# Performance work log

Measured on AMD Instinct MI355X. Metric: run time of the kernel, lower is better.

The kernel has to match this reference:

```python
import jax, jax.numpy as jnp
import numpy as np

HID, NH, HD = 1024, 16, 64
B, S = 2, 2048


def _gammas(nh):
    # gammas = 1 - exp(linspace(log(1/512), log(1/32), nh))
    lin = np.linspace(np.log(1.0 / 512.0), np.log(1.0 / 32.0), nh)
    return jnp.asarray(1.0 - np.exp(lin), dtype=jnp.float32)


def setup_inputs() -> dict:
    key = jax.random.key(0)
    ks = jax.random.split(key, 6)
    x = jax.random.normal(ks[0], (B, S, HID), dtype=jnp.float32)
    # Per-head retention projection weights (Retention has its own q/k/v of [head_size, head_size])
    wq = jax.random.normal(ks[1], (NH, HD, HD), dtype=jnp.float32) / HD
    wk = jax.random.normal(ks[2], (NH, HD, HD), dtype=jnp.float32) / HD
    wv = jax.random.normal(ks[3], (NH, HD, HD), dtype=jnp.float32) / HD
    w1 = jax.random.normal(ks[4], (HID, HID), dtype=jnp.float32) / HID
    w2 = jax.random.normal(ks[5], (HID, HID), dtype=jnp.float32) / HID
    gn_scale = jnp.ones((HID,), dtype=jnp.float32)
    gn_bias = jnp.zeros((HID,), dtype=jnp.float32)
    return {"x": x, "wq": wq, "wk": wk, "wv": wv, "w1": w1, "w2": w2,
            "gn_scale": gn_scale, "gn_bias": gn_bias}


def reference(x, wq, wk, wv, w1, w2, gn_scale, gn_bias):
    b, s, h = x.shape
    nh, hd = wq.shape[0], wq.shape[1]
    gammas = _gammas(nh)  # [nh]

    xh = x.reshape(b, s, nh, hd)
    q = jnp.einsum('bsnd,nde->bsne', xh, wq)
    k = jnp.einsum('bsnd,nde->bsne', xh, wk)
    v = jnp.einsum('bsnd,nde->bsne', xh, wv)

    # causal decay mask D[n, s, t] = gamma_n ** (s - t) for s >= t else 0
    idx = jnp.arange(s)
    diff = (idx[:, None] - idx[None, :]).astype(jnp.float32)  # [s, s]
    safe = jnp.maximum(diff, 0.0)
    D = jnp.where(diff >= 0,
                  jnp.exp(safe[None] * jnp.log(gammas)[:, None, None]),
                  0.0)  # [nh, s, s]

    scores = jnp.einsum('bsnd,btnd->bnst', q, k) * D[None]      # [b, nh, s, s]
    ret = jnp.einsum('bnst,btnd->bsnd', scores, v)              # [b, s, nh, hd]

    # GroupNorm(num_groups=nh, num_channels=h) over flattened [b*s, h]:
    # normalize within each head-group of hd channels, affine per-channel, eps=1e-5
    mean = ret.mean(axis=-1, keepdims=True)
    var = ret.var(axis=-1, keepdims=True)
    norm = (ret - mean) / jnp.sqrt(var + 1e-5)
    norm = norm.reshape(b, s, h) * gn_scale + gn_bias

    gate = jnp.matmul(x, w1)
    out = gate * jax.nn.sigmoid(gate) + norm  # swish-gated branch + retention
    return jnp.matmul(out, w2)
```

## Files before the change

kernel.cpp:

```cpp
#include <hip/hip_runtime.h>

#define HIDD 1024
#define NHH  16
#define HDD  64
#define BBB  2
#define SSS  2048
#define BS   (BBB * SSS)

typedef __attribute__((ext_vector_type(8))) _Float16 half8;
typedef __attribute__((ext_vector_type(4))) _Float16 half4;
typedef __attribute__((ext_vector_type(4))) float    f32x4;

#define LSCALE 2048.0f
#define LINV   (1.0f / 2048.0f)

static __device__ __forceinline__ f32x4 mfma16h(half8 a, half8 b, f32x4 c) {
    return __builtin_amdgcn_mfma_f32_16x16x32_f16(a, b, c, 0, 0, 0);
}

static __device__ __forceinline__ void split2h(float v, _Float16& h, _Float16& l) {
    h = (_Float16)v;
    l = (_Float16)((v - (float)h) * LSCALE);
}

static __device__ __forceinline__ void gl_lds16(const _Float16* g, _Float16* l) {
    __builtin_amdgcn_global_load_lds(
        (const __attribute__((address_space(1))) unsigned int*)g,
        (__attribute__((address_space(3))) unsigned int*)l,
        16, 0, 0);
}

__global__ __launch_bounds__(256) void k_wprep(const float* __restrict__ wq,
                                               const float* __restrict__ wk,
                                               const float* __restrict__ wv,
                                               _Float16* __restrict__ WTh,
                                               _Float16* __restrict__ WTl) {
    const int blk = blockIdx.x;
    const int mat = blk >> 4, n = blk & 15;
    const float* src = (mat == 0 ? wq : mat == 1 ? wk : wv) + (size_t)n * 4096;
    for (int c = threadIdx.x; c < 4096; c += 256) {
        int e = c >> 6, d = c & 63;
        float v = src[d * 64 + e];
        _Float16 h, l;
        split2h(v, h, l);
        WTh[(size_t)blk * 4096 + c] = h;
        WTl[(size_t)blk * 4096 + c] = l;
    }
}

__global__ __launch_bounds__(512) void k_proj_mfma(const float* __restrict__ x,
                                                   const _Float16* __restrict__ WTh,
                                                   const _Float16* __restrict__ WTl,
                                                   _Float16* __restrict__ Qh, _Float16* __restrict__ Ql,
                                                   _Float16* __restrict__ Kh, _Float16* __restrict__ Kl,
                                                   _Float16* __restrict__ VTh, _Float16* __restrict__ VTl) {
    const int n  = blockIdx.y;
    const int R0 = blockIdx.x * 128;
    const int tid = threadIdx.x;
    const int w = tid >> 6, lane = tid & 63;
    const int hi = lane >> 4, lo = lane & 15;

    __shared__ __align__(16) _Float16 smem[27648];

    half8 ah[2], al[2];
#pragma unroll
    for (int kf = 0; kf < 2; kf++) {
        const float* xp = x + (size_t)(R0 + 16 * w + lo) * HIDD + n * HDD + kf * 32 + 8 * hi;
        float4 v0 = *(const float4*)xp;
        float4 v1 = *(const float4*)(xp + 4);
        float vv[8] = { v0.x, v0.y, v0.z, v0.w, v1.x, v1.y, v1.z, v1.w };
#pragma unroll
        for (int j = 0; j < 8; ++j) {
            _Float16 h, l;
            split2h(vv[j], h, l);
            ah[kf][j] = h; al[kf][j] = l;
        }
    }

    for (int c = tid; c < 3072; c += 512) {
        int m = c >> 10, rest = c & 1023, hl = rest >> 9, cc = rest & 511;
        int r = cc >> 3, j8 = (cc & 7) << 3;
        const _Float16* src = (hl ? WTl : WTh) + ((size_t)(m * NHH + n)) * 4096 + r * 64 + j8;
        *(half8*)&smem[(m * 2 + hl) * 4608 + r * 72 + j8] = *(const half8*)src;
    }
    __syncthreads();

    const int bq = R0 >> 11;
    const int sr = R0 & 2047;
    const size_t bn = (size_t)(bq * NHH + n);
    float vkeep[4][4][2];

    for (int mat = 0; mat < 3; ++mat) {
        const _Float16* bh_base = smem + (mat * 2 + 0) * 4608;
        const _Float16* bl_base = smem + (mat * 2 + 1) * 4608;
        f32x4 a0[4], a1[4];
#pragma unroll
        for (int eb = 0; eb < 4; ++eb) {
            a0[eb] = (f32x4){0.f, 0.f, 0.f, 0.f};
            a1[eb] = (f32x4){0.f, 0.f, 0.f, 0.f};
        }
#pragma unroll
        for (int eb = 0; eb < 4; ++eb) {
            half8 bh0 = *(const half8*)&bh_base[(16 * eb + lo) * 72 + 8 * hi];
            half8 bh1 = *(const half8*)&bh_base[(16 * eb + lo) * 72 + 32 + 8 * hi];
            half8 bl0 = *(const half8*)&bl_base[(16 * eb + lo) * 72 + 8 * hi];
            half8 bl1 = *(const half8*)&bl_base[(16 * eb + lo) * 72 + 32 + 8 * hi];
            a0[eb] = mfma16h(ah[0], bh0, a0[eb]);
            a0[eb] = mfma16h(ah[1], bh1, a0[eb]);
            a1[eb] = mfma16h(ah[0], bl0, a1[eb]);
            a1[eb] = mfma16h(al[0], bh0, a1[eb]);
            a1[eb] = mfma16h(ah[1], bl1, a1[eb]);
            a1[eb] = mfma16h(al[1], bh1, a1[eb]);
        }

        if (mat < 2) {
            _Float16* Dh = (mat == 0) ? Qh : Kh;
            _Float16* Dl = (mat == 0) ? Ql : Kl;
#pragma unroll
            for (int eb = 0; eb < 4; ++eb)
#pragma unroll
                for (int r = 0; r < 4; ++r) {
                    int gr = R0 + 16 * w + 4 * hi + r;
                    int s = gr & 2047;
                    float val = a0[eb][r] + a1[eb][r] * LINV;
                    _Float16 h, l;
                    split2h(val, h, l);
                    size_t idx = (bn * SSS + s) * HDD + 16 * eb + lo;
                    Dh[idx] = h; Dl[idx] = l;
                }
        } else {
#pragma unroll
            for (int eb = 0; eb < 4; ++eb)
#pragma unroll
                for (int r = 0; r < 4; ++r) {
                    vkeep[eb][r][0] = a0[eb][r];
                    vkeep[eb][r][1] = a1[eb][r];
                }
        }
    }

    __syncthreads();
    _Float16* tbh = smem;
    _Float16* tbl = smem + 8704;
#pragma unroll
    for (int eb = 0; eb < 4; ++eb)
#pragma unroll
        for (int r = 0; r < 4; ++r) {
            int rl = 16 * w + 4 * hi + r;
            int ch = 16 * eb + lo;
            _Float16 h, l;
            split2h(vkeep[eb][r][0] + vkeep[eb][r][1] * LINV, h, l);
            tbh[ch * 136 + rl] = h;
            tbl[ch * 136 + rl] = l;
        }
    __syncthreads();
    for (int c = tid; c < 1024; c += 512) {
        int ch = c >> 4, s8 = (c & 15) << 3;
        int a64 = s8 & 64;
        int s0 = s8 & 63;
        int basePerm = a64 + (s0 & 32) + ((s0 >> 3) & 3) * 4;
        const _Float16* th = &tbh[ch * 136];
        const _Float16* tl = &tbl[ch * 136];
        half4 h0 = *(const half4*)(th + basePerm);
        half4 h1 = *(const half4*)(th + basePerm + 16);
        half4 l0 = *(const half4*)(tl + basePerm);
        half4 l1 = *(const half4*)(tl + basePerm + 16);
        half8 oh = {h0[0], h0[1], h0[2], h0[3], h1[0], h1[1], h1[2], h1[3]};
        half8 ol = {l0[0], l0[1], l0[2], l0[3], l1[0], l1[1], l1[2], l1[3]};
        size_t gi = (bn * HDD + ch) * SSS + sr + s8;
        *(half8*)(VTh + gi) = oh;
        *(half8*)(VTl + gi) = ol;
    }
}

__global__ __launch_bounds__(256) void k_ret_mfma(const _Float16* __restrict__ Qh, const _Float16* __restrict__ Ql,
                                                  const _Float16* __restrict__ Kh, const _Float16* __restrict__ Kl,
                                                  const _Float16* __restrict__ VTh, const _Float16* __restrict__ VTl,
                                                  const float* __restrict__ gns,
                                                  const float* __restrict__ gnb,
                                                  float* __restrict__ normb) {
    const int n = blockIdx.y, b = blockIdx.z;
    const int qt = (n < 8) ? ((int)gridDim.x - 1 - (int)blockIdx.x) : (int)blockIdx.x;
    const int tid = threadIdx.x;
    const int w = tid >> 6, lane = tid & 63;
    const int hi = lane >> 4, lo = lane & 15;

    const double l512 = -6.2383246250395075;
    const double l32  = -3.4657359027997265;
    double lin = l512 + (double)n * (l32 - l512) / 15.0;
    float gamma = (float)(1.0 - exp(lin));
    float l2g = log2f(gamma);
    int dmax = (int)(16.0f / (-l2g)) + 1;

    const int qb = qt * 64;
    const int qw = qb + 16 * w;
    int stb_start = (qb > dmax) ? ((qb - dmax) >> 5) : 0;
    const int stb_end  = 2 * qt + 1;
    const int stb_diag = qw >> 5;

    const size_t bn = (size_t)(b * NHH + n);
    const _Float16* Qhp = Qh + bn * SSS * HDD;
    const _Float16* Qlp = Ql + bn * SSS * HDD;
    const _Float16* Khp = Kh + bn * SSS * HDD;
    const _Float16* Klp = Kl + bn * SSS * HDD;
    const _Float16* Vhp = VTh + bn * HDD * SSS;
    const _Float16* Vlp = VTl + bn * HDD * SSS;

    half8 qfh[2], qfl[2];
#pragma unroll
    for (int kf = 0; kf < 2; kf++) {
        size_t o = (size_t)(qw + lo) * HDD + kf * 32 + 8 * hi;
        qfh[kf] = *(const half8*)(Qhp + o);
        qfl[kf] = *(const half8*)(Qlp + o);
    }

    f32x4 acc0[4], acc1[4];
#pragma unroll
    for (int e = 0; e < 4; e++) {
        acc0[e] = (f32x4){0.f, 0.f, 0.f, 0.f};
        acc1[e] = (f32x4){0.f, 0.f, 0.f, 0.f};
    }

    __shared__ __align__(16) _Float16 ksh[4096];
    __shared__ __align__(16) _Float16 ksl[4096];
    __shared__ __align__(16) _Float16 vsh[4096];
    __shared__ __align__(16) _Float16 vsl[4096];

    const _Float16* sg = (w == 0) ? Khp : (w == 1) ? Klp : (w == 2) ? Vhp : Vlp;
    _Float16* slds = (w == 0) ? ksh : (w == 1) ? ksl : (w == 2) ? vsh : vsl;
    size_t goff;
    if (w < 2) goff = (size_t)(lane >> 3) * HDD + (size_t)((((lane & 7) ^ ((lane >> 3) & 7))) << 3);
    else       goff = (size_t)(lane >> 2) * SSS + (size_t)((((lane & 3) ^ ((lane >> 3) & 3))) << 3);

    auto issue = [&](int tbase, int pb) {
        _Float16* Lb = slds + pb * 2048;
        if (w < 2) {
#pragma unroll
            for (int i = 0; i < 4; ++i)
                gl_lds16(sg + (size_t)(tbase + 8 * i) * HDD + goff, Lb + i * 512);
        } else {
#pragma unroll
            for (int i = 0; i < 4; ++i)
                gl_lds16(sg + (size_t)(16 * i) * SSS + tbase + goff, Lb + i * 512);
        }
    };

    const int ks0 = ((hi ^ (lo & 7)) << 3);
    const int ks1 = (((4 + hi) ^ (lo & 7)) << 3);
    const int vs0 = ((hi ^ ((lo >> 1) & 3)) << 3);

    float ftile = exp2f((float)(qw + lo - stb_start * 32) * l2g);
    const float gi16   = exp2f(-16.0f * l2g);
    const float ginv32 = exp2f(-32.0f * l2g);
    float f4[4];
#pragma unroll
    for (int r = 0; r < 4; ++r) f4[r] = exp2f(-(float)(4 * hi + r) * l2g);

    int pb = 0;
    issue(stb_start * 32, 0);
    __syncthreads();

    for (int stb = stb_start; stb <= stb_end; ++stb) {
        const int tbase = stb * 32;
        if (stb < stb_end) issue(tbase + 32, pb ^ 1);

        const bool active = (tbase <= qw + 15) && (tbase + 31 >= qw - dmax);
        if (active) {
            const bool dm = (stb == stb_diag);
            const _Float16* kh_ = &ksh[pb * 2048];
            const _Float16* kl_ = &ksl[pb * 2048];
            const _Float16* vh_ = &vsh[pb * 2048];
            const _Float16* vl_ = &vsl[pb * 2048];
            _Float16 ph4[2][4], pl4[2][4];
#pragma unroll
            for (int tt = 0; tt < 2; ++tt) {
                int rb = (16 * tt + lo) * 64;
                half8 kh0 = *(const half8*)&kh_[rb + ks0];
                half8 kh1 = *(const half8*)&kh_[rb + ks1];
                half8 kl0 = *(const half8*)&kl_[rb + ks0];
                half8 kl1 = *(const half8*)&kl_[rb + ks1];
                f32x4 s0 = (f32x4){0.f, 0.f, 0.f, 0.f};
                f32x4 s1 = (f32x4){0.f, 0.f, 0.f, 0.f};
                s0 = mfma16h(kh0, qfh[0], s0);
                s0 = mfma16h(kh1, qfh[1], s0);
                s1 = mfma16h(kl0, qfh[0], s1);
                s1 = mfma16h(kh0, qfl[0], s1);
                s1 = mfma16h(kl1, qfh[1], s1);
                s1 = mfma16h(kh1, qfl[1], s1);
                const float g = tt ? ftile * gi16 : ftile;
#pragma unroll
                for (int r = 0; r < 4; r++) {
                    float p = (s0[r] + s1[r] * LINV) * (g * f4[r]);
                    if (dm) {
                        int diff = (qw + lo) - (tbase + 16 * tt + 4 * hi + r);
                        if (diff < 0) p = 0.0f;
                    }
                    split2h(p, ph4[tt][r], pl4[tt][r]);
                }
            }
            half8 pfh = (half8){ph4[0][0], ph4[0][1], ph4[0][2], ph4[0][3],
                                ph4[1][0], ph4[1][1], ph4[1][2], ph4[1][3]};
            half8 pfl = (half8){pl4[0][0], pl4[0][1], pl4[0][2], pl4[0][3],
                                pl4[1][0], pl4[1][1], pl4[1][2], pl4[1][3]};
#pragma unroll
            for (int e = 0; e < 4; e++) {
                int vb = (16 * e + lo) * 32 + vs0;
                half8 vh0 = *(const half8*)&vh_[vb];
                half8 vl0 = *(const half8*)&vl_[vb];
                acc0[e] = mfma16h(pfh, vh0, acc0[e]);
                acc1[e] = mfma16h(pfh, vl0, acc1[e]);
                acc1[e] = mfma16h(pfl, vh0, acc1[e]);
            }
        }
        ftile *= ginv32;
        __syncthreads();
        pb ^= 1;
    }

    f32x4 accf[4];
#pragma unroll
    for (int e = 0; e < 4; e++)
#pragma unroll
        for (int r = 0; r < 4; r++)
            accf[e][r] = acc0[e][r] + acc1[e][r] * LINV;

    float s[4], sq[4];
#pragma unroll
    for (int r = 0; r < 4; r++) {
        s[r] = 0.f; sq[r] = 0.f;
#pragma unroll
        for (int e = 0; e < 4; e++) { float v = accf[e][r]; s[r] += v; sq[r] += v * v; }
    }
#pragma unroll
    for (int mask = 1; mask < 16; mask <<= 1)
#pragma unroll
        for (int r = 0; r < 4; r++) {
            s[r]  += __shfl_xor(s[r],  mask);
            sq[r] += __shfl_xor(sq[r], mask);
        }
#pragma unroll
    for (int e = 0; e < 4; e++)
#pragma unroll
        for (int r = 0; r < 4; r++) {
            float mean = s[r] * (1.0f / 64.0f);
            float var  = sq[r] * (1.0f / 64.0f) - mean * mean;
            float rstd = rsqrtf(var + 1e-5f);
            int ch = 16 * e + lo;
            int sg2 = qw + 4 * hi + r;
            float nv = (accf[e][r] - mean) * rstd;
            nv = nv * gns[n * 64 + ch] + gnb[n * 64 + ch];
            normb[((size_t)b * SSS + sg2) * HIDD + n * 64 + ch] = nv;
        }
}

__global__ __launch_bounds__(256) void k_cvt_h(const float* __restrict__ src,
                                               _Float16* __restrict__ dst) {
    int i = blockIdx.x * 256 + threadIdx.x;
    float4 v = reinterpret_cast<const float4*>(src)[i];
    half4 o = { (_Float16)v.x, (_Float16)v.y, (_Float16)v.z, (_Float16)v.w };
    reinterpret_cast<half4*>(dst)[i] = o;
}

__global__ __launch_bounds__(256) void k_tr_h(const float* __restrict__ src,
                                              _Float16* __restrict__ dst,
                                              int K, int N) {
    __shared__ float ls[32][33];
    int kb = blockIdx.y * 32, nb = blockIdx.x * 32;
    int tx = threadIdx.x & 31, ty = threadIdx.x >> 5;
#pragma unroll
    for (int i = 0; i < 4; i++) {
        int r = ty + 8 * i;
        ls[r][tx] = src[(size_t)(kb + r) * N + nb + tx];
    }
    __syncthreads();
#pragma unroll
    for (int i = 0; i < 4; i++) {
        int r = ty + 8 * i;
        dst[(size_t)(nb + r) * K + kb + tx] = (_Float16)ls[tx][r];
    }
}

template <int MODE>
__global__ __launch_bounds__(256) void k_gemm_h(const _Float16* __restrict__ A,
                                                const _Float16* __restrict__ Bt,
                                                const float* __restrict__ normb,
                                                _Float16* __restrict__ Y,
                                                float* __restrict__ Out) {
    const int Rb = blockIdx.x * 128, Cb = blockIdx.y * 128;
    const int tid = threadIdx.x, w = tid >> 6, lane = tid & 63;
    const int hi = lane >> 4, lo = lane & 15;
    const int wm = w >> 1, wn = w & 1;

    __shared__ __align__(16) _Float16 as[128 * 40];
    __shared__ __align__(16) _Float16 bs[128 * 40];

    f32x4 acc[4][4];
#pragma unroll
    for (int m = 0; m < 4; m++)
#pragma unroll
        for (int nn = 0; nn < 4; nn++) acc[m][nn] = (f32x4){0.f, 0.f, 0.f, 0.f};

    half8 pre[4];
    auto g_issue = [&](int kk) {
#pragma unroll
        for (int i = 0; i < 4; ++i) {
            int c = tid + (i << 8);
            int which = c >> 9, cc = c & 511, row = cc >> 2, j8 = (cc & 3) << 3;
            const _Float16* src = (which == 0)
                ? A  + (size_t)(Rb + row) * HIDD + kk * 32 + j8
                : Bt + (size_t)(Cb + row) * HIDD + kk * 32 + j8;
            pre[i] = *(const half8*)src;
        }
    };
    auto g_commit = [&]() {
#pragma unroll
        for (int i = 0; i < 4; ++i) {
            int c = tid + (i << 8);
            int which = c >> 9, cc = c & 511, row = cc >> 2, j8 = (cc & 3) << 3;
            _Float16* dst = (which == 0) ? as : bs;
            *(half8*)&dst[row * 40 + j8] = pre[i];
        }
    };

    g_issue(0);
    g_commit();
    __syncthreads();

    for (int kk = 0; kk < 32; ++kk) {
        if (kk < 31) g_issue(kk + 1);
        half8 af[4], bf[4];
#pragma unroll
        for (int m = 0; m < 4; m++)
            af[m] = *(const half8*)&as[(64 * wm + 16 * m + lo) * 40 + 8 * hi];
#pragma unroll
        for (int nn = 0; nn < 4; nn++)
            bf[nn] = *(const half8*)&bs[(64 * wn + 16 * nn + lo) * 40 + 8 * hi];
#pragma unroll
        for (int m = 0; m < 4; m++)
#pragma unroll
            for (int nn = 0; nn < 4; nn++)
                acc[m][nn] = mfma16h(af[m], bf[nn], acc[m][nn]);
        __syncthreads();
        if (kk < 31) g_commit();
        __syncthreads();
    }

#pragma unroll
    for (int m = 0; m < 4; m++)
#pragma unroll
        for (int nn = 0; nn < 4; nn++)
#pragma unroll
            for (int r = 0; r < 4; r++) {
                int row = Rb + 64 * wm + 16 * m + 4 * hi + r;
                int col = Cb + 64 * wn + 16 * nn + lo;
                float v = acc[m][nn][r];
                size_t idx = (size_t)row * HIDD + col;
                if (MODE == 0) {
                    float sw = v / (1.0f + expf(-v));
                    float y = sw + normb[idx];
                    Y[idx] = (_Float16)y;
                } else {
                    Out[idx] = v;
                }
            }
}

extern "C" void kernel_launch(void* const* d_in, const int* in_sizes, int n_in,
                              void* d_out, int out_size, void* d_ws, size_t ws_size,
                              hipStream_t stream) {
    const float* x   = (const float*)d_in[0];
    const float* wq  = (const float*)d_in[1];
    const float* wk  = (const float*)d_in[2];
    const float* wv  = (const float*)d_in[3];
    const float* w1  = (const float*)d_in[4];
    const float* w2  = (const float*)d_in[5];
    const float* gns = (const float*)d_in[6];
    const float* gnb = (const float*)d_in[7];
    float* out = (float*)d_out;

    char* base = (char*)d_ws;
    size_t off = 0;
    auto carve = [&](size_t bytes) -> void* {
        void* p = base + off;
        off += (bytes + 255) & ~(size_t)255;
        return p;
    };
    _Float16* Qh  = (_Float16*)carve((size_t)BS * HIDD * 2);
    _Float16* Ql  = (_Float16*)carve((size_t)BS * HIDD * 2);
    _Float16* Kh  = (_Float16*)carve((size_t)BS * HIDD * 2);
    _Float16* Kl  = (_Float16*)carve((size_t)BS * HIDD * 2);
    _Float16* VTh = (_Float16*)carve((size_t)BS * HIDD * 2);
    _Float16* VTl = (_Float16*)carve((size_t)BS * HIDD * 2);
    float*    normb = (float*)carve((size_t)BS * HIDD * 4);
    _Float16* WTh = (_Float16*)normb;
    _Float16* WTl = WTh + (size_t)48 * 4096;
    _Float16* xh  = Qh;
    _Float16* w1t = Kh;
    _Float16* w2t = Kh + (size_t)HIDD * HIDD;
    _Float16* yh  = VTh;
    (void)ws_size; (void)in_sizes; (void)n_in; (void)out_size;

    k_wprep<<<48, 256, 0, stream>>>(wq, wk, wv, WTh, WTl);
    k_proj_mfma<<<dim3(BS / 128, NHH), 512, 0, stream>>>(x, WTh, WTl,
                                                         Qh, Ql, Kh, Kl, VTh, VTl);
    k_ret_mfma<<<dim3(SSS / 64, NHH, BBB), 256, 0, stream>>>(Qh, Ql, Kh, Kl, VTh, VTl,
                                                             gns, gnb, normb);
    k_cvt_h<<<(BS * HIDD) / 4 / 256, 256, 0, stream>>>(x, xh);
    k_tr_h<<<dim3(32, 32), 256, 0, stream>>>(w1, w1t, HIDD, HIDD);
    k_tr_h<<<dim3(32, 32), 256, 0, stream>>>(w2, w2t, HIDD, HIDD);
    k_gemm_h<0><<<dim3(BS / 128, HIDD / 128), 256, 0, stream>>>(xh, w1t, normb, yh, nullptr);
    k_gemm_h<1><<<dim3(BS / 128, HIDD / 128), 256, 0, stream>>>(yh, w2t, nullptr, nullptr, out);
}
```

Before: 168.9 us.

## Use direct global-to-LDS loads with XOR swizzle and BK=64 in fp16 GEMM

Replaces the register-staged global→LDS prefetch (issue/commit with padded 40-stride rows) with direct global-to-LDS 16-byte loads (gl_lds16), an XOR-swizzled unpadded 64-wide layout, and a doubled K tile of 64 per iteration. This is meant to cut register pressure, VGPR round-trips and loop iterations, and to avoid bank conflicts without padding. The trade-off is that the software prefetch overlap is lost: each iteration now syncs, loads, syncs, then computes, with no double-buffering.

```diff
diff --git a/kernel.cpp b/kernel.cpp
--- a/kernel.cpp
+++ b/kernel.cpp
@@ -391,8 +391,8 @@
     const int hi = lane >> 4, lo = lane & 15;
     const int wm = w >> 1, wn = w & 1;
 
-    __shared__ __align__(16) _Float16 as[128 * 40];
-    __shared__ __align__(16) _Float16 bs[128 * 40];
+    __shared__ __align__(16) _Float16 as[128 * 64];
+    __shared__ __align__(16) _Float16 bs[128 * 64];
 
     f32x4 acc[4][4];
 #pragma unroll
@@ -400,49 +400,45 @@
 #pragma unroll
         for (int nn = 0; nn < 4; nn++) acc[m][nn] = (f32x4){0.f, 0.f, 0.f, 0.f};
 
-    half8 pre[4];
-    auto g_issue = [&](int kk) {
-#pragma unroll
-        for (int i = 0; i < 4; ++i) {
-            int c = tid + (i << 8);
-            int which = c >> 9, cc = c & 511, row = cc >> 2, j8 = (cc & 3) << 3;
-            const _Float16* src = (which == 0)
-                ? A  + (size_t)(Rb + row) * HIDD + kk * 32 + j8
-                : Bt + (size_t)(Cb + row) * HIDD + kk * 32 + j8;
-            pre[i] = *(const half8*)src;
-        }
-    };
-    auto g_commit = [&]() {
-#pragma unroll
-        for (int i = 0; i < 4; ++i) {
-            int c = tid + (i << 8);
-            int which = c >> 9, cc = c & 511, row = cc >> 2, j8 = (cc & 3) << 3;
-            _Float16* dst = (which == 0) ? as : bs;
-            *(half8*)&dst[row * 40 + j8] = pre[i];
-        }
-    };
-
-    g_issue(0);
-    g_commit();
-    __syncthreads();
-
-    for (int kk = 0; kk < 32; ++kk) {
-        if (kk < 31) g_issue(kk + 1);
-        half8 af[4], bf[4];
+    const _Float16* gM = (w < 2) ? (A + (size_t)(Rb + 64 * (w & 1)) * HIDD)
+                                 : (Bt + (size_t)(Cb + 64 * (w & 1)) * HIDD);
+    _Float16* gL = ((w < 2) ? as : bs) + (w & 1) * 64 * 64;
+    const size_t gofs = (size_t)(lane >> 3) * HIDD
+                      + (size_t)((((lane & 7) ^ ((lane >> 3) & 7))) << 3);
+
+    int rsw[2];
+#pragma unroll
+    for (int kf = 0; kf < 2; kf++) rsw[kf] = ((4 * kf + hi) ^ (lo & 7)) << 3;
+
+    for (int kk = 0; kk < 16; ++kk) {
+        __syncthreads();
+#pragma unroll
+        for (int i = 0; i < 8; ++i)
+            gl_lds16(gM + (size_t)(8 * i) * HIDD + kk * 64 + gofs, gL + i * 512);
+        __syncthreads();
+
+        half8 af[4][2], bf[4][2];
+#pragma unroll
+        for (int m = 0; m < 4; m++) {
+            int row = 64 * wm + 16 * m + lo;
+#pragma unroll
+            for (int kf = 0; kf < 2; kf++)
+                af[m][kf] = *(const half8*)&as[row * 64 + rsw[kf]];
+        }
+#pragma unroll
+        for (int nn = 0; nn < 4; nn++) {
+            int row = 64 * wn + 16 * nn + lo;
+#pragma unroll
+            for (int kf = 0; kf < 2; kf++)
+                bf[nn][kf] = *(const half8*)&bs[row * 64 + rsw[kf]];
+        }
 #pragma unroll
         for (int m = 0; m < 4; m++)
-            af[m] = *(const half8*)&as[(64 * wm + 16 * m + lo) * 40 + 8 * hi];
-#pragma unroll
-        for (int nn = 0; nn < 4; nn++)
-            bf[nn] = *(const half8*)&bs[(64 * wn + 16 * nn + lo) * 40 + 8 * hi];
-#pragma unroll
-        for (int m = 0; m < 4; m++)
-#pragma unroll
-            for (int nn = 0; nn < 4; nn++)
-                acc[m][nn] = mfma16h(af[m], bf[nn], acc[m][nn]);
-        __syncthreads();
-        if (kk < 31) g_commit();
-        __syncthreads();
+#pragma unroll
+            for (int nn = 0; nn < 4; nn++) {
+                acc[m][nn] = mfma16h(af[m][0], bf[nn][0], acc[m][nn]);
+                acc[m][nn] = mfma16h(af[m][1], bf[nn][1], acc[m][nn]);
+            }
     }
 
 #pragma unroll
```

Result: no change. 166.1 us (-1.7%).
